# Kernel tuning notes

Measured on AMD Instinct MI355X. Metric: run time of the kernel, lower is better.

Reference implementation:

```python
import jax, jax.numpy as jnp
import numpy as np

IN_DIM = 128
OUT_DIM = 128
NUM_INTERVALS = 8
SPLINE_ORDER = 3
BATCH = 1024


def make_grids():
    # domain [-1, 1] for every (in, out) pair, extended by spline_order knots each side
    step = 2.0 / NUM_INTERVALS
    G = NUM_INTERVALS + 2 * SPLINE_ORDER + 1
    g = (-1.0 - SPLINE_ORDER * step) + jnp.arange(G, dtype=jnp.float32) * step  # [G]
    return jnp.broadcast_to(g, (IN_DIM, OUT_DIM, G))


def setup_inputs() -> dict:
    key = jax.random.key(0)
    k1, k2, k3 = jax.random.split(key, 3)
    x = jax.random.normal(k1, (BATCH, IN_DIM), dtype=jnp.float32)
    n_cp = NUM_INTERVALS + SPLINE_ORDER
    control_points = 0.1 * jax.random.normal(k2, (IN_DIM, OUT_DIM, n_cp), dtype=jnp.float32)
    scaling_factors = np.sqrt(2.0 / OUT_DIM).astype(np.float32) * jax.random.normal(
        k3, (IN_DIM, OUT_DIM), dtype=jnp.float32)
    grids = make_grids()
    return {"x": x, "control_points": control_points,
            "scaling_factors": scaling_factors, "grids": grids}


def bspline_bases(x, grids, k):
    # Bottom-up Cox-de-Boor DP (identical recurrence to the naive top-down version).
    # x: [B, in], grids: [in, out, G] -> returns all degree-k bases [B, in, out, G-1-k]
    ex = x[:, :, None, None]          # [B, in, 1, 1]
    t = grids[None]                   # [1, in, out, G]
    B = ((t[..., :-1] <= ex) & (ex < t[..., 1:])).astype(x.dtype)  # degree 0
    for d in range(1, k + 1):
        tl  = t[..., : -(d + 1)]      # t[i]
        tr  = t[..., d:-1]            # t[i+d]
        tl1 = t[..., 1:-d]            # t[i+1]
        tr1 = t[..., d + 1:]          # t[i+d+1]
        B = (ex - tl) / (tr - tl) * B[..., :-1] + (tr1 - ex) / (tr1 - tl1) * B[..., 1:]
    return B


def reference(x, control_points, scaling_factors, grids):
    Bk = bspline_bases(x, grids, SPLINE_ORDER)                 # [B, in, out, n_cp]
    spline = jnp.einsum('biog,iog->bio', Bk, control_points)    # [B, in, out]
    res = scaling_factors[None] * (jax.nn.silu(x)[:, :, None] + spline)
    return jnp.sum(res, axis=1).astype(jnp.float32)             # [B, out]
```

## Files before the change

kernel.cpp:

```cpp
#include <hip/hip_runtime.h>
#include <math.h>


#define IN_DIM   128
#define OUT_DIM  128
#define NCP      11
#define FS       12
#define KTOT     (IN_DIM * FS)
#define MT       16
#define NSTEP    (KTOT / 32)
#define ASTR     1544

typedef __attribute__((ext_vector_type(8))) short short8;
typedef __attribute__((ext_vector_type(4))) float f32x4;

static __device__ __forceinline__ unsigned short f2bf(float f) {
    unsigned int x = __float_as_uint(f);
    unsigned int r = (x + 0x7fffu + ((x >> 16) & 1u)) >> 16;
    return (unsigned short)r;
}

__global__ __launch_bounds__(256)
void kan_prep(const float* __restrict__ CP, const float* __restrict__ SF,
              unsigned short* __restrict__ Wz)
{
    const int idx  = blockIdx.x * 256 + threadIdx.x;
    const int s    = idx >> 9;
    const int rem  = idx & 511;
    const int t    = rem >> 6;
    const int lane = rem & 63;
    const int o     = 16 * t + (lane & 15);
    const int kbase = 32 * s + 8 * (lane >> 4);

    unsigned int q[4];
    #pragma unroll
    for (int jj = 0; jj < 4; ++jj) {
        unsigned short lo = 0, hi = 0;
        #pragma unroll
        for (int half = 0; half < 2; ++half) {
            const int k = kbase + 2 * jj + half;
            const int i = k / 12;
            const int g = k - 12 * i;
            const float sf = SF[i * OUT_DIM + o];
            const float v  = (g == NCP) ? sf : sf * CP[(i * OUT_DIM + o) * NCP + g];
            if (half == 0) lo = f2bf(v); else hi = f2bf(v);
        }
        q[jj] = (unsigned int)lo | ((unsigned int)hi << 16);
    }
    *(uint4*)&Wz[idx * 8] = make_uint4(q[0], q[1], q[2], q[3]);
}

__global__ __launch_bounds__(256)
void kan_gemm(const float* __restrict__ X, const float* __restrict__ GR,
              const unsigned short* __restrict__ Wz, float* __restrict__ OUT)
{
    __shared__ __align__(16) unsigned short A[MT * ASTR];

    const int tid = threadIdx.x;
    const int m0  = blockIdx.x * MT;

    const float t0   = GR[0];
    const float invh = 1.0f / (GR[1] - t0);

    #pragma unroll
    for (int kq = 0; kq < (MT * IN_DIM) / 256; ++kq) {
        const int p_ = tid + kq * 256;
        const int r  = p_ >> 7;
        const int i  = p_ & (IN_DIM - 1);

        const float x  = X[(m0 + r) * IN_DIM + i];
        const float xr = (x - t0) * invh;
        const float pf = floorf(xr);
        const int   p  = (int)pf;
        const float u  = xr - pf;
        const float um = 1.0f - u;
        const float u2 = u * u, u3 = u2 * u;
        const float c0 = um * um * um * (1.0f / 6.0f);
        const float c1 = (3.0f * u3 - 6.0f * u2 + 4.0f) * (1.0f / 6.0f);
        const float c2 = (-3.0f * u3 + 3.0f * u2 + 3.0f * u + 1.0f) * (1.0f / 6.0f);
        const float c3 = u3 * (1.0f / 6.0f);
        const float silu = x / (1.0f + __expf(-x));

        const bool ok = (p >= 0) && (p <= 13);
        const int  j0 = ok ? (p - 3) : -999;
        const int  pp = ok ? p : -999;

        unsigned short us[FS];
        #pragma unroll
        for (int g = 0; g < NCP; ++g) {
            float v = (g == j0)     ? c0
                    : (g == j0 + 1) ? c1
                    : (g == j0 + 2) ? c2
                    : (g == pp)     ? c3 : 0.0f;
            us[g] = f2bf(v);
        }
        us[NCP] = f2bf(silu);

        uint2* dst = (uint2*)&A[r * ASTR + i * FS];
        dst[0] = make_uint2((unsigned)us[0] | ((unsigned)us[1] << 16),
                            (unsigned)us[2] | ((unsigned)us[3] << 16));
        dst[1] = make_uint2((unsigned)us[4] | ((unsigned)us[5] << 16),
                            (unsigned)us[6] | ((unsigned)us[7] << 16));
        dst[2] = make_uint2((unsigned)us[8] | ((unsigned)us[9] << 16),
                            (unsigned)us[10] | ((unsigned)us[11] << 16));
    }
    __syncthreads();

    const int lane = tid & 63;
    const int w    = tid >> 6;
    const int row  = lane & 15;
    const int quad = lane >> 4;

    f32x4 acc0 = (f32x4){0.f, 0.f, 0.f, 0.f};
    f32x4 acc1 = (f32x4){0.f, 0.f, 0.f, 0.f};

    const unsigned short* ab = &A[row * ASTR];
    #pragma unroll 8
    for (int s = 0; s < NSTEP; ++s) {
        const short8 a  = *(const short8*)(ab + s * 32 + 8 * quad);
        const unsigned short* b = Wz + (size_t)((s * 8 + 2 * w) * 64 + lane) * 8;
        const short8 bA = *(const short8*)(b);
        const short8 bB = *(const short8*)(b + 64 * 8);
        acc0 = __builtin_amdgcn_mfma_f32_16x16x32_bf16(a, bA, acc0, 0, 0, 0);
        acc1 = __builtin_amdgcn_mfma_f32_16x16x32_bf16(a, bB, acc1, 0, 0, 0);
    }

    #pragma unroll
    for (int q = 0; q < 4; ++q) {
        const int rr = m0 + 4 * quad + q;
        OUT[rr * OUT_DIM + 16 * (2 * w + 0) + row] = acc0[q];
        OUT[rr * OUT_DIM + 16 * (2 * w + 1) + row] = acc1[q];
    }
}

extern "C" void kernel_launch(void* const* d_in, const int* in_sizes, int n_in,
                              void* d_out, int out_size, void* d_ws, size_t ws_size,
                              hipStream_t stream) {
    const float* x  = (const float*)d_in[0];
    const float* cp = (const float*)d_in[1];
    const float* sf = (const float*)d_in[2];
    const float* gr = (const float*)d_in[3];
    float* out = (float*)d_out;

    const int batch = in_sizes[0] / IN_DIM;

    unsigned short* Wz = (unsigned short*)d_ws;

    kan_prep<<<(NSTEP * 8 * 64) / 256, 256, 0, stream>>>(cp, sf, Wz);
    kan_gemm<<<batch / MT, 256, 0, stream>>>(x, gr, Wz, out);
}
```

Baseline: 79.68 us.

## Split GEMM over N blocks and K across waves with register-prefetched B

```diff
diff --git a/kernel.cpp b/kernel.cpp
--- a/kernel.cpp
+++ b/kernel.cpp
@@ -8,7 +8,9 @@
 #define FS       12
 #define KTOT     (IN_DIM * FS)
 #define MT       16
+#define NT       32
 #define NSTEP    (KTOT / 32)
+#define WSTEP    (NSTEP / 4)
 #define ASTR     1544
 
 typedef __attribute__((ext_vector_type(8))) short short8;
@@ -58,6 +60,23 @@
 
     const int tid = threadIdx.x;
     const int m0  = blockIdx.x * MT;
+    const int nb  = blockIdx.y;
+    const int n0  = NT * nb;
+
+    const int lane = tid & 63;
+    const int w    = tid >> 6;
+    const int r15  = lane & 15;
+    const int quad = lane >> 4;
+
+    short8 breg0[WSTEP], breg1[WSTEP];
+    #pragma unroll
+    for (int sl = 0; sl < WSTEP; ++sl) {
+        const int s = WSTEP * w + sl;
+        const unsigned short* b =
+            Wz + (size_t)(((s * 8) + 2 * nb) * 64 + lane) * 8;
+        breg0[sl] = *(const short8*)(b);
+        breg1[sl] = *(const short8*)(b + 64 * 8);
+    }
 
     const float t0   = GR[0];
     const float invh = 1.0f / (GR[1] - t0);
@@ -106,30 +125,37 @@
     }
     __syncthreads();
 
-    const int lane = tid & 63;
-    const int w    = tid >> 6;
-    const int row  = lane & 15;
-    const int quad = lane >> 4;
-
     f32x4 acc0 = (f32x4){0.f, 0.f, 0.f, 0.f};
     f32x4 acc1 = (f32x4){0.f, 0.f, 0.f, 0.f};
 
-    const unsigned short* ab = &A[row * ASTR];
-    #pragma unroll 8
-    for (int s = 0; s < NSTEP; ++s) {
-        const short8 a  = *(const short8*)(ab + s * 32 + 8 * quad);
-        const unsigned short* b = Wz + (size_t)((s * 8 + 2 * w) * 64 + lane) * 8;
-        const short8 bA = *(const short8*)(b);
-        const short8 bB = *(const short8*)(b + 64 * 8);
-        acc0 = __builtin_amdgcn_mfma_f32_16x16x32_bf16(a, bA, acc0, 0, 0, 0);
-        acc1 = __builtin_amdgcn_mfma_f32_16x16x32_bf16(a, bB, acc1, 0, 0, 0);
+    const unsigned short* ab = &A[r15 * ASTR];
+    #pragma unroll
+    for (int sl = 0; sl < WSTEP; ++sl) {
+        const int s = WSTEP * w + sl;
+        const short8 a = *(const short8*)(ab + s * 32 + 8 * quad);
+        acc0 = __builtin_amdgcn_mfma_f32_16x16x32_bf16(a, breg0[sl], acc0, 0, 0, 0);
+        acc1 = __builtin_amdgcn_mfma_f32_16x16x32_bf16(a, breg1[sl], acc1, 0, 0, 0);
     }
 
+    __syncthreads();
+    float* red = (float*)A;
     #pragma unroll
     for (int q = 0; q < 4; ++q) {
-        const int rr = m0 + 4 * quad + q;
-        OUT[rr * OUT_DIM + 16 * (2 * w + 0) + row] = acc0[q];
-        OUT[rr * OUT_DIM + 16 * (2 * w + 1) + row] = acc1[q];
+        const int m = quad * 4 + q;
+        red[w * 528 + m * 33 + r15]      = acc0[q];
+        red[w * 528 + m * 33 + 16 + r15] = acc1[q];
+    }
+    __syncthreads();
+
+    #pragma unroll
+    for (int e = tid; e < MT * NT; e += 256) {
+        const int m = e >> 5;
+        const int n = e & 31;
+        float v = 0.0f;
+        #pragma unroll
+        for (int ww = 0; ww < 4; ++ww)
+            v += red[ww * 528 + m * 33 + n];
+        OUT[(m0 + m) * OUT_DIM + n0 + n] = v;
     }
 }
 
@@ -147,5 +173,6 @@
     unsigned short* Wz = (unsigned short*)d_ws;
 
     kan_prep<<<(NSTEP * 8 * 64) / 256, 256, 0, stream>>>(cp, sf, Wz);
-    kan_gemm<<<batch / MT, 256, 0, stream>>>(x, gr, Wz, out);
+    dim3 grid(batch / MT, OUT_DIM / NT);
+    kan_gemm<<<grid, 256, 0, stream>>>(x, gr, Wz, out);
 }
```

Result: faster. 69.33 us (-13.0%).
